# Kernel tuning notes

Measured on AMD Instinct MI355X. Metric: run time of the kernel, lower is better.

## Reference

```python
import jax, jax.numpy as jnp
import numpy as np

N, H, F = 768, 8, 16
HF = H * F            # 128, also node_in
NODE_IN = 128
EIN, EOUT = 64, 64
E = 24576
NEG = -1e9
SLOPE = 0.2
EPS = 1e-5


def leaky(x):
    return jnp.where(x >= 0, x, SLOPE * x)


def batchnorm(x, g, b):
    # BatchNorm1d with track_running_stats=False: always uses batch stats (biased var)
    m = x.mean(0)
    v = x.var(0)
    return g * (x - m) / jnp.sqrt(v + EPS) + b


def setup_inputs() -> dict:
    key = jax.random.key(0)
    ks = jax.random.split(key, 25)
    s = 0.1
    inp = {
        "in_nodes_features": jax.random.normal(ks[0], (N, NODE_IN), jnp.float32),
        "in_edges_features": jax.random.normal(ks[1], (N, N, EIN), jnp.float32),
        "connectivity_mask": jnp.where(jax.random.uniform(ks[2], (N, N)) < 0.05, 0.0, NEG).astype(jnp.float32),
        "sparse_edge_features": jax.random.normal(ks[3], (E, EIN), jnp.float32),
        "sparse_edge_indexs": jax.random.randint(ks[4], (E, 2), 0, N, jnp.int64) if jax.config.jax_enable_x64 else jax.random.randint(ks[4], (E, 2), 0, N, jnp.int32),
        "Wp": jax.random.normal(ks[5], (HF, NODE_IN), jnp.float32) * s,          # linear_proj
        "Wp2": jax.random.normal(ks[6], (HF, EIN), jnp.float32) * s,             # linear_proj2
        "bp2": jax.random.normal(ks[7], (HF,), jnp.float32) * s,
        "score_src": jax.random.normal(ks[8], (1, H, F), jnp.float32) * s,
        "score_tgt": jax.random.normal(ks[9], (1, H, F), jnp.float32) * s,
        "score_edge": jax.random.normal(ks[10], (1, 1, H, F), jnp.float32) * s,
        "Wskip": jax.random.normal(ks[11], (HF, NODE_IN), jnp.float32) * s,      # skip_proj
        "node_bias": jax.random.normal(ks[12], (HF,), jnp.float32) * s,
        "bn_node_g": jnp.ones((HF,), jnp.float32),
        "bn_node_b": jnp.zeros((HF,), jnp.float32),
        "Wf1": jax.random.normal(ks[13], (EOUT, EIN), jnp.float32) * s,
        "bf1": jax.random.normal(ks[14], (EOUT,), jnp.float32) * s,
        "Wf2": jax.random.normal(ks[15], (EOUT, HF), jnp.float32) * s,
        "Wf3": jax.random.normal(ks[16], (EOUT, 2 * EOUT), jnp.float32) * s,
        "Wf4": jax.random.normal(ks[17], (EOUT, EIN), jnp.float32) * s,
        "bf4": jax.random.normal(ks[18], (EOUT,), jnp.float32) * s,
        "Wes": jax.random.normal(ks[19], (EOUT, EIN), jnp.float32) * s,          # edge_skip_proj
        "bn_edge_g": jnp.ones((EOUT,), jnp.float32),
        "bn_edge_b": jnp.zeros((EOUT,), jnp.float32),
    }
    return inp


def reference(in_nodes_features, in_edges_features, connectivity_mask, sparse_edge_features,
              sparse_edge_indexs, Wp, Wp2, bp2, score_src, score_tgt, score_edge, Wskip,
              node_bias, bn_node_g, bn_node_b, Wf1, bf1, Wf2, Wf3, Wf4, bf4, Wes,
              bn_edge_g, bn_edge_b):
    x, edges, mask = in_nodes_features, in_edges_features, connectivity_mask
    # --- node (GAT w/ edge-score bias) path (dropout=0 -> identity) ---
    np_proj = (x @ Wp.T).reshape(N, H, F)                                  # [N,H,F]
    ep = leaky((edges @ Wp2.T) + bp2).reshape(N, N, H, F)                  # [N,N,H,F]
    ss = jnp.sum(np_proj * score_src[0], -1)                               # [N,H]
    st = jnp.sum(np_proj * score_tgt[0], -1)                               # [N,H]
    se = jnp.sum(ep * score_edge[0, 0], -1)                                # [N,N,H]
    scores = leaky(ss.T[:, :, None] + st.T[:, None, :])                    # [H,N,N]
    escores = leaky(jnp.transpose(se, (2, 0, 1)))                          # [H,N,N]
    attn = jax.nn.softmax(scores + escores + mask[None], axis=-1)          # [H,N,N]
    outn = jnp.einsum('hij,jhf->ihf', attn, np_proj)                       # [N,H,F]
    outn = outn + (x @ Wskip.T).reshape(N, H, F)                           # skip (F != node_in)
    outn = outn.reshape(N, HF)                                             # concat heads
    outn = jax.nn.elu(batchnorm(outn, bn_node_g, bn_node_b) + node_bias)
    # --- edge learning path ---
    si, sj = sparse_edge_indexs[:, 0], sparse_edge_indexs[:, 1]
    m_ij = leaky(sparse_edge_features @ Wf1.T + bf1)                       # [E,EOUT]
    d = outn[si] - outn[sj]                                                # gather instead of dense NxN diff
    r_ij = leaky((d * d) @ Wf2.T)                                          # [E,EOUT]
    oe = jnp.concatenate([m_ij, r_ij], -1) @ Wf3.T
    oe = oe + sparse_edge_features @ Wes.T
    oe = jax.nn.elu(batchnorm(oe, bn_edge_g, bn_edge_b))
    ie = (edges @ Wf4.T + bf4) * jax.nn.softmax(mask, axis=-1)[..., None]  # [N,N,EOUT]
    ie = ie.at[si, sj].set(oe)
    return (outn, ie, mask, oe, sparse_edge_indexs)
```

## Files before the change

### kernel.cpp

```cpp
#include <hip/hip_runtime.h>
#include <math.h>

#define NN 768
#define H 8
#define F 16
#define HF 128
#define EIN 64
#define EOUT 64
#define E_EDGES 24576
#define SLOPE 0.2f
#define EPS 1e-5f

__device__ __forceinline__ float leaky(float x){ return x >= 0.f ? x : SLOPE*x; }
__device__ __forceinline__ float elu1(float x){ return x > 0.f ? x : expm1f(x); }

__global__ void k_proj(const float* __restrict__ x, const float* __restrict__ Wp,
                       const float* __restrict__ Wskip, const float* __restrict__ ssrc,
                       const float* __restrict__ stgt,
                       float* __restrict__ npj, float* __restrict__ ss, float* __restrict__ st,
                       float* __restrict__ outn_pre){
  __shared__ float xsh[HF];
  __shared__ float ps[HF], pt[HF];
  int i = blockIdx.x, c = threadIdx.x;
  xsh[c] = x[i*HF + c];
  __syncthreads();
  float a = 0.f, b = 0.f;
  #pragma unroll 4
  for(int k=0;k<HF;k++){ float xv = xsh[k]; a += xv*Wp[c*HF+k]; b += xv*Wskip[c*HF+k]; }
  npj[i*HF+c] = a;
  outn_pre[i*HF+c] = b;
  ps[c] = a*ssrc[c]; pt[c] = a*stgt[c];
  __syncthreads();
  if(c < H){
    float s1=0.f, s2=0.f;
    #pragma unroll
    for(int f=0; f<F; f++){ s1 += ps[c*F+f]; s2 += pt[c*F+f]; }
    ss[i*H+c]=s1; st[i*H+c]=s2;
  }
}

__global__ void k_list(const float* __restrict__ mask, int* __restrict__ lists, int* __restrict__ cnt){
  int w = threadIdx.x >> 6, lane = threadIdx.x & 63;
  int i = blockIdx.x*4 + w;
  int base = 0;
  const float* mrow = mask + (size_t)i*NN;
  int* lrow = lists + (size_t)i*NN;
  for(int t=0;t<12;t++){
    int j = t*64 + lane;
    bool un = (mrow[j] == 0.0f);
    unsigned long long b = __ballot(un);
    if(un) lrow[base + __popcll(b & ((1ull<<lane)-1ull))] = j;
    base += (int)__popcll(b);
  }
  if(base == 0){
    for(int t=0;t<12;t++) lrow[t*64+lane] = t*64+lane;
    base = NN;
  }
  if(lane==0) cnt[i] = base;
}

__global__ __launch_bounds__(256,4) void k_logits_sparse(
    const float* __restrict__ edges, const float* __restrict__ Wp2,
    const float* __restrict__ bp2, const float* __restrict__ sce,
    const float* __restrict__ ss, const float* __restrict__ st,
    const float* __restrict__ mask,
    const int* __restrict__ lists, const int* __restrict__ cnt,
    float* __restrict__ logitc){
  __shared__ float4 wsh[HF*16];
  __shared__ float4 esh[4][2][16];
  __shared__ float bsh[HF], scsh[HF];
  int i = blockIdx.x, tid = threadIdx.x;
  const float4* W4 = (const float4*)Wp2;
  #pragma unroll
  for(int t=0;t<8;t++) wsh[tid + t*256] = W4[tid + t*256];
  if(tid < HF){ bsh[tid]=bp2[tid]; scsh[tid]=sce[tid]; }
  __syncthreads();
  int w = tid>>6, lane = tid&63;
  int n = cnt[i];
  float ss0 = ss[i*H + (lane>>4)];
  float ss1 = ss[i*H + 4 + (lane>>4)];
  const int* lrow = lists + (size_t)i*NN;
  for(int s0 = w*2; s0 < n; s0 += 8){
    int s1 = s0 + 1;
    int j0 = lrow[s0];
    int j1 = lrow[(s1 < n) ? s1 : s0];
    if(lane < 32){
      int which = lane >> 4, k4 = lane & 15;
      int jj = which ? j1 : j0;
      esh[w][which][k4] = ((const float4*)(edges + ((size_t)i*NN + jj)*EIN))[k4];
    }
    asm volatile("s_waitcnt lgkmcnt(0) vmcnt(0)" ::: "memory");
    __builtin_amdgcn_sched_barrier(0);
    float a00=0.f,a01=0.f,a10=0.f,a11=0.f;
    #pragma unroll
    for(int t=0;t<16;t++){
      int q = t ^ (lane & 15);
      float4 e0 = esh[w][0][q];
      float4 e1 = esh[w][1][q];
      float4 w0 = wsh[lane*16 + q];
      float4 w1 = wsh[(lane+64)*16 + q];
      a00 += e0.x*w0.x + e0.y*w0.y + e0.z*w0.z + e0.w*w0.w;
      a01 += e1.x*w0.x + e1.y*w0.y + e1.z*w0.z + e1.w*w0.w;
      a10 += e0.x*w1.x + e0.y*w1.y + e0.z*w1.z + e0.w*w1.w;
      a11 += e1.x*w1.x + e1.y*w1.y + e1.z*w1.z + e1.w*w1.w;
    }
    float p;
    p = a00 + bsh[lane];    float v0  = leaky(p)*scsh[lane];
    p = a01 + bsh[lane];    float v0b = leaky(p)*scsh[lane];
    p = a10 + bsh[lane+64]; float v1  = leaky(p)*scsh[lane+64];
    p = a11 + bsh[lane+64]; float v1b = leaky(p)*scsh[lane+64];
    #pragma unroll
    for(int o=1;o<16;o<<=1){
      v0 += __shfl_xor(v0,o); v0b += __shfl_xor(v0b,o);
      v1 += __shfl_xor(v1,o); v1b += __shfl_xor(v1b,o);
    }
    if((lane & 15) == 0){
      int h = lane >> 4;
      float m0 = mask[(size_t)i*NN + j0];
      logitc[((size_t)i*H + h)*NN + s0]     = leaky(v0) + leaky(ss0 + st[j0*H + h]) + m0;
      logitc[((size_t)i*H + h + 4)*NN + s0] = leaky(v1) + leaky(ss1 + st[j0*H + h + 4]) + m0;
      if(s1 < n){
        float m1 = mask[(size_t)i*NN + j1];
        logitc[((size_t)i*H + h)*NN + s1]     = leaky(v0b) + leaky(ss0 + st[j1*H + h]) + m1;
        logitc[((size_t)i*H + h + 4)*NN + s1] = leaky(v1b) + leaky(ss1 + st[j1*H + h + 4]) + m1;
      }
    }
  }
}

__global__ void k_softmax_c(float* __restrict__ logitc, const int* __restrict__ cnt){
  int i = blockIdx.x;
  int g = threadIdx.x >> 5, l = threadIdx.x & 31;
  int n = cnt[i];
  float* row = logitc + ((size_t)i*H + g)*NN;
  float m = -1e30f;
  for(int s=l; s<n; s+=32) m = fmaxf(m, row[s]);
  #pragma unroll
  for(int o=1;o<32;o<<=1) m = fmaxf(m, __shfl_xor(m, o, 32));
  float sum = 0.f;
  for(int s=l; s<n; s+=32){ float e = expf(row[s]-m); row[s]=e; sum+=e; }
  #pragma unroll
  for(int o=1;o<32;o<<=1) sum += __shfl_xor(sum, o, 32);
  float inv = 1.f/sum;
  for(int s=l; s<n; s+=32) row[s] *= inv;
}

__global__ void k_einsum_c(const float* __restrict__ attnc, const int* __restrict__ lists,
                           const int* __restrict__ cnt, const float* __restrict__ npj,
                           float* __restrict__ opre){
  int i = blockIdx.x, c = threadIdx.x;
  int h = c >> 4;
  int n = cnt[i];
  const int* lrow = lists + (size_t)i*NN;
  const float* arow = attnc + ((size_t)i*H + h)*NN;
  float acc = opre[i*HF + c];
  #pragma unroll 4
  for(int s=0; s<n; s++) acc += arow[s] * npj[lrow[s]*HF + c];
  opre[i*HF+c] = acc;
}

__global__ void k_bn_node_stats(const float* __restrict__ outn_pre, float* __restrict__ stats){
  int c = threadIdx.x & 127, half = threadIdx.x >> 7;
  int r0 = blockIdx.x*16 + half*8;
  float s1=0.f, s2=0.f;
  #pragma unroll
  for(int r=0;r<8;r++){ float v = outn_pre[(r0+r)*HF + c]; s1+=v; s2+=v*v; }
  __shared__ float l1[256], l2[256];
  l1[threadIdx.x]=s1; l2[threadIdx.x]=s2;
  __syncthreads();
  if(threadIdx.x < 128){
    s1 = l1[threadIdx.x] + l1[threadIdx.x+128];
    s2 = l2[threadIdx.x] + l2[threadIdx.x+128];
    atomicAdd(&stats[c], s1); atomicAdd(&stats[HF + c], s2);
  }
}

__global__ void k_bn_node_apply(const float* __restrict__ outn_pre, const float* __restrict__ stats,
                                const float* __restrict__ g, const float* __restrict__ b,
                                const float* __restrict__ nbias, float* __restrict__ outn){
  int idx = blockIdx.x*256 + threadIdx.x;
  int c = idx & 127;
  float m  = stats[c] * (1.f/NN);
  float var = stats[HF+c]*(1.f/NN) - m*m;
  float xv = outn_pre[idx];
  float y = g[c]*(xv - m)/sqrtf(var + EPS) + b[c] + nbias[c];
  outn[idx] = elu1(y);
}

__global__ __launch_bounds__(256,1) void k_sparse_oe(
    const float* __restrict__ sef, const int* __restrict__ eidx,
    const float* __restrict__ outn,
    const float* __restrict__ Wf1, const float* __restrict__ bf1,
    const float* __restrict__ Wf2, const float* __restrict__ Wf3,
    const float* __restrict__ Wes,
    float* __restrict__ oe_pre, float* __restrict__ stats){
  __shared__ float w1[64*65];
  __shared__ float w2[64*129];
  __shared__ float w3[64*129];
  __shared__ float we[64*65];
  __shared__ float b1sh[64];
  __shared__ float sefsh[4][64];
  __shared__ float ddsh[4][128];
  __shared__ float msh[4][64], rsh[4][64];
  __shared__ float r1[256], r2[256];
  int tid = threadIdx.x;
  for(int idx = tid; idx < 64*64; idx += 256){ int o = idx>>6, k = idx&63; w1[o*65+k] = Wf1[idx]; we[o*65+k] = Wes[idx]; }
  for(int idx = tid; idx < 64*128; idx += 256){ int o = idx>>7, k = idx&127; w2[o*129+k] = Wf2[idx]; w3[o*129+k] = Wf3[idx]; }
  if(tid<64) b1sh[tid] = bf1[tid];
  int e0 = blockIdx.x * 96;
  float s1 = 0.f, s2 = 0.f;
  int ee = tid >> 6, o = tid & 63;
  for(int eg=0; eg<24; eg++){
    int ebase = e0 + eg*4;
    { int k = tid & 63, e4 = tid >> 6; sefsh[e4][k] = sef[(ebase+e4)*64 + k]; }
    #pragma unroll
    for(int t=0;t<2;t++){
      int idx = tid + t*256; int e4 = idx >> 7, c = idx & 127;
      int ed = ebase + e4;
      int si = eidx[ed*2], sj = eidx[ed*2+1];
      float d = outn[si*HF + c] - outn[sj*HF + c];
      ddsh[e4][c] = d*d;
    }
    __syncthreads();
    float m = b1sh[o], r = 0.f, oes = 0.f;
    #pragma unroll 4
    for(int k=0;k<64;k++){ float sv = sefsh[ee][k]; m += sv*w1[o*65+k]; oes += sv*we[o*65+k]; }
    #pragma unroll 4
    for(int c=0;c<128;c++){ r += ddsh[ee][c]*w2[o*129+c]; }
    m = leaky(m); r = leaky(r);
    msh[ee][o] = m; rsh[ee][o] = r;
    __syncthreads();
    float oe = oes;
    #pragma unroll 4
    for(int k=0;k<64;k++){ oe += msh[ee][k]*w3[o*129+k] + rsh[ee][k]*w3[o*129+64+k]; }
    oe_pre[(size_t)(ebase+ee)*64 + o] = oe;
    s1 += oe; s2 += oe*oe;
    __syncthreads();
  }
  r1[tid] = s1; r2[tid] = s2;
  __syncthreads();
  if(tid < 64){
    float a1 = r1[tid] + r1[tid+64] + r1[tid+128] + r1[tid+192];
    float a2 = r2[tid] + r2[tid+64] + r2[tid+128] + r2[tid+192];
    atomicAdd(&stats[256 + tid], a1);
    atomicAdd(&stats[320 + tid], a2);
  }
}

__global__ void k_bn_edge_apply(const float* __restrict__ oe_pre, const float* __restrict__ stats,
                                const float* __restrict__ g, const float* __restrict__ b,
                                float* __restrict__ oe_out){
  int idx = blockIdx.x*256 + threadIdx.x;
  int o = idx & 63;
  float m = stats[256+o] * (1.f/E_EDGES);
  float var = stats[320+o]*(1.f/E_EDGES) - m*m;
  float xv = oe_pre[idx];
  float y = g[o]*(xv-m)/sqrtf(var+EPS) + b[o];
  oe_out[idx] = elu1(y);
}

__global__ __launch_bounds__(256) void k_ie_fill(
    const float* __restrict__ edges, const float* __restrict__ mask,
    const float* __restrict__ Wf4, const float* __restrict__ bf4,
    float* __restrict__ ie){
  __shared__ float w4[64*65];
  __shared__ float b4sh[64];
  __shared__ int list[NN];
  __shared__ int lcnt;
  int i = blockIdx.x, tid = threadIdx.x;
  if(tid==0) lcnt = 0;
  for(int idx=tid; idx<64*64; idx+=256){ int o=idx>>6,k=idx&63; w4[o*65+k]=Wf4[idx]; }
  if(tid<64) b4sh[tid]=bf4[tid];
  __syncthreads();
  for(int t=0;t<3;t++){
    int j = tid + t*256;
    if(mask[i*NN+j] == 0.0f){ int p = atomicAdd(&lcnt,1); list[p]=j; }
  }
  __syncthreads();
  int cnt = lcnt;
  float inv;
  if(cnt == 0){
    for(int t=0;t<3;t++) list[tid+t*256] = tid+t*256;
    cnt = NN; inv = 1.0f/NN;
    __syncthreads();
  } else inv = 1.0f/cnt;
  int o = tid & 63, jj4 = tid >> 6;
  for(int base=0; base<cnt; base+=4){
    int li = base + jj4;
    if(li < cnt){
      int j = list[li];
      const float* er = edges + ((size_t)i*NN + j)*EIN;
      float acc = b4sh[o];
      #pragma unroll 8
      for(int k=0;k<64;k++) acc += er[k]*w4[o*65+k];
      ie[((size_t)i*NN + j)*EIN + o] = acc * inv;
    }
  }
}

__global__ void k_winner(const int* __restrict__ eidx, int* __restrict__ winner){
  int e = blockIdx.x*256 + threadIdx.x;
  if(e < E_EDGES){
    int si = eidx[e*2], sj = eidx[e*2+1];
    atomicMax(&winner[si*NN+sj], e);
  }
}
__global__ void k_scatter(const int* __restrict__ eidx, const int* __restrict__ winner,
                          const float* __restrict__ oe, float* __restrict__ ie){
  int idx = blockIdx.x*256 + threadIdx.x;
  int e = idx >> 6, o = idx & 63;
  int si = eidx[e*2], sj = eidx[e*2+1];
  if(winner[si*NN+sj] == e) ie[((size_t)si*NN+sj)*EIN + o] = oe[(size_t)e*64+o];
}

__global__ void k_idxf(const int* __restrict__ eidx, float* __restrict__ outf){
  int idx = blockIdx.x*256 + threadIdx.x;
  if(idx < E_EDGES*2) outf[idx] = (float)eidx[idx];
}

extern "C" void kernel_launch(void* const* d_in, const int* in_sizes, int n_in,
                              void* d_out, int out_size, void* d_ws, size_t ws_size,
                              hipStream_t stream){
  (void)in_sizes; (void)n_in; (void)out_size; (void)d_ws; (void)ws_size;
  const float* x     = (const float*)d_in[0];
  const float* edges = (const float*)d_in[1];
  const float* mask  = (const float*)d_in[2];
  const float* sef   = (const float*)d_in[3];
  const int*   eidx  = (const int*)d_in[4];
  const float* Wp    = (const float*)d_in[5];
  const float* Wp2   = (const float*)d_in[6];
  const float* bp2   = (const float*)d_in[7];
  const float* ssrc  = (const float*)d_in[8];
  const float* stgt  = (const float*)d_in[9];
  const float* sce   = (const float*)d_in[10];
  const float* Wskip = (const float*)d_in[11];
  const float* nbias = (const float*)d_in[12];
  const float* bng   = (const float*)d_in[13];
  const float* bnb   = (const float*)d_in[14];
  const float* Wf1   = (const float*)d_in[15];
  const float* bf1   = (const float*)d_in[16];
  const float* Wf2   = (const float*)d_in[17];
  const float* Wf3   = (const float*)d_in[18];
  const float* Wf4   = (const float*)d_in[19];
  const float* bf4   = (const float*)d_in[20];
  const float* Wes   = (const float*)d_in[21];
  const float* beg   = (const float*)d_in[22];
  const float* beb   = (const float*)d_in[23];

  float* out      = (float*)d_out;
  float* out_outn = out;
  float* out_ie   = out + 98304;
  float* out_mask = out + 37847040;
  float* out_oe   = out + 38436864;
  float* out_idx  = out + 40009728;

  float* s_logitc = out_ie;
  float* s_npj    = out_ie + 4718592;
  float* s_ss     = s_npj + 98304;
  float* s_st     = s_ss + 6144;
  float* s_opre   = s_st + 6144;
  float* s_oepre  = s_opre + 98304;
  float* s_stats  = s_oepre + 1572864;
  int*   s_lists  = (int*)(s_stats + 512);
  int*   s_cnt    = s_lists + 2359296;
  int*   winner   = (int*)out_mask;

  hipMemsetAsync(s_stats, 0, 512*sizeof(float), stream);
  hipMemsetAsync(winner, 0xFF, (size_t)NN*NN*sizeof(int), stream);

  k_list<<<NN/4, 256, 0, stream>>>(mask, s_lists, s_cnt);
  k_proj<<<NN, 128, 0, stream>>>(x, Wp, Wskip, ssrc, stgt, s_npj, s_ss, s_st, s_opre);
  k_logits_sparse<<<NN, 256, 0, stream>>>(edges, Wp2, bp2, sce, s_ss, s_st, mask, s_lists, s_cnt, s_logitc);
  k_softmax_c<<<NN, 256, 0, stream>>>(s_logitc, s_cnt);
  k_einsum_c<<<NN, 128, 0, stream>>>(s_logitc, s_lists, s_cnt, s_npj, s_opre);
  k_bn_node_stats<<<48, 256, 0, stream>>>(s_opre, s_stats);
  k_bn_node_apply<<<384, 256, 0, stream>>>(s_opre, s_stats, bng, bnb, nbias, out_outn);
  k_sparse_oe<<<E_EDGES/96, 256, 0, stream>>>(sef, eidx, out_outn, Wf1, bf1, Wf2, Wf3, Wes, s_oepre, s_stats);
  k_bn_edge_apply<<<6144, 256, 0, stream>>>(s_oepre, s_stats, beg, beb, out_oe);
  hipMemsetAsync(out_ie, 0, (size_t)NN*NN*EIN*sizeof(float), stream);
  k_ie_fill<<<NN, 256, 0, stream>>>(edges, mask, Wf4, bf4, out_ie);
  k_winner<<<96, 256, 0, stream>>>(eidx, winner);
  k_scatter<<<6144, 256, 0, stream>>>(eidx, winner, out_oe, out_ie);
  hipMemcpyAsync(out_mask, mask, (size_t)NN*NN*sizeof(float), hipMemcpyDeviceToDevice, stream);
  k_idxf<<<192, 256, 0, stream>>>(eidx, out_idx);
}
```

Before: 542.4 us.

## Replace per-row projection and fused edge MLP with register-tiled GEMM kernels

Rewrites the node projection as a tiled GEMM kernel with swizzled shared-memory float4 tiles, and moves the attention score reduction into a separate shuffle-based kernel. The monolithic per-edge MLP kernel, which ran with low occupancy and three barriers per four edges, is split into three GEMM-style kernels plus a separate BN-stats reduction. This raises parallelism and register reuse, at the cost of extra intermediate buffers in global memory and more kernel launches.

```diff
diff --git a/kernel.cpp b/kernel.cpp
--- a/kernel.cpp
+++ b/kernel.cpp
@@ -14,29 +14,60 @@
 __device__ __forceinline__ float leaky(float x){ return x >= 0.f ? x : SLOPE*x; }
 __device__ __forceinline__ float elu1(float x){ return x > 0.f ? x : expm1f(x); }
 
-__global__ void k_proj(const float* __restrict__ x, const float* __restrict__ Wp,
-                       const float* __restrict__ Wskip, const float* __restrict__ ssrc,
-                       const float* __restrict__ stgt,
-                       float* __restrict__ npj, float* __restrict__ ss, float* __restrict__ st,
-                       float* __restrict__ outn_pre){
-  __shared__ float xsh[HF];
-  __shared__ float ps[HF], pt[HF];
+__global__ __launch_bounds__(256,3) void k_proj2(
+    const float* __restrict__ x, const float* __restrict__ Wp, const float* __restrict__ Wskip,
+    float* __restrict__ npj, float* __restrict__ opre){
+  __shared__ float4 Bsh[64*32];
+  __shared__ float4 Ash[32*32];
+  int tid = threadIdx.x;
+  int tile = blockIdx.x >> 2, chunk = blockIdx.x & 3;
+  int i0 = tile*32;
+  const float4* Wsrc = (const float4*)((chunk < 2 ? Wp : Wskip) + (size_t)(chunk & 1)*64*HF);
+  const float4* X4 = (const float4*)(x + (size_t)i0*HF);
+  #pragma unroll
+  for(int t=0;t<8;t++){
+    int fi = tid + t*256;
+    int n = fi >> 5, s = fi & 31;
+    Bsh[n*32 + (s ^ ((n>>2)&15))] = Wsrc[fi];
+  }
+  #pragma unroll
+  for(int t=0;t<4;t++){
+    int fi = tid + t*256;
+    int e = fi >> 5, s = fi & 31;
+    Ash[e*32 + (s ^ ((e>>1)&15))] = X4[fi];
+  }
+  __syncthreads();
+  int og = tid & 15, eg = tid >> 4;
+  int o0 = og*4, eb = eg*2;
+  float acc[2][4] = {};
+  #pragma unroll
+  for(int s=0;s<32;s++){
+    float4 a0 = Ash[(eb+0)*32 + (s ^ (((eb+0)>>1)&15))];
+    float4 a1 = Ash[(eb+1)*32 + (s ^ (((eb+1)>>1)&15))];
+    #pragma unroll
+    for(int oo=0;oo<4;oo++){
+      float4 b = Bsh[(o0+oo)*32 + (s ^ (((o0+oo)>>2)&15))];
+      acc[0][oo] += a0.x*b.x + a0.y*b.y + a0.z*b.z + a0.w*b.w;
+      acc[1][oo] += a1.x*b.x + a1.y*b.y + a1.z*b.z + a1.w*b.w;
+    }
+  }
+  float* dst = (chunk < 2) ? npj : opre;
+  int col = (chunk & 1)*64 + o0;
+  #pragma unroll
+  for(int ee=0;ee<2;ee++){
+    float4 v; v.x=acc[ee][0]; v.y=acc[ee][1]; v.z=acc[ee][2]; v.w=acc[ee][3];
+    *(float4*)(dst + (size_t)(i0+eb+ee)*HF + col) = v;
+  }
+}
+
+__global__ void k_scores(const float* __restrict__ npj, const float* __restrict__ ssrc,
+                         const float* __restrict__ stgt, float* __restrict__ ss, float* __restrict__ st){
   int i = blockIdx.x, c = threadIdx.x;
-  xsh[c] = x[i*HF + c];
-  __syncthreads();
-  float a = 0.f, b = 0.f;
-  #pragma unroll 4
-  for(int k=0;k<HF;k++){ float xv = xsh[k]; a += xv*Wp[c*HF+k]; b += xv*Wskip[c*HF+k]; }
-  npj[i*HF+c] = a;
-  outn_pre[i*HF+c] = b;
-  ps[c] = a*ssrc[c]; pt[c] = a*stgt[c];
-  __syncthreads();
-  if(c < H){
-    float s1=0.f, s2=0.f;
-    #pragma unroll
-    for(int f=0; f<F; f++){ s1 += ps[c*F+f]; s2 += pt[c*F+f]; }
-    ss[i*H+c]=s1; st[i*H+c]=s2;
-  }
+  float p = npj[i*HF + c];
+  float v1 = p*ssrc[c], v2 = p*stgt[c];
+  #pragma unroll
+  for(int o=1;o<16;o<<=1){ v1 += __shfl_xor(v1,o); v2 += __shfl_xor(v2,o); }
+  if((c&15)==0){ ss[i*H + (c>>4)] = v1; st[i*H + (c>>4)] = v2; }
 }
 
 __global__ void k_list(const float* __restrict__ mask, int* __restrict__ lists, int* __restrict__ cnt){
@@ -187,63 +218,171 @@
   outn[idx] = elu1(y);
 }
 
-__global__ __launch_bounds__(256,1) void k_sparse_oe(
-    const float* __restrict__ sef, const int* __restrict__ eidx,
-    const float* __restrict__ outn,
-    const float* __restrict__ Wf1, const float* __restrict__ bf1,
-    const float* __restrict__ Wf2, const float* __restrict__ Wf3,
-    const float* __restrict__ Wes,
-    float* __restrict__ oe_pre, float* __restrict__ stats){
-  __shared__ float w1[64*65];
-  __shared__ float w2[64*129];
-  __shared__ float w3[64*129];
-  __shared__ float we[64*65];
+__global__ __launch_bounds__(256,3) void k_mlp_a(
+    const float* __restrict__ sef, const float* __restrict__ Wf1, const float* __restrict__ bf1,
+    const float* __restrict__ Wes, float* __restrict__ m_out, float* __restrict__ oes_out){
+  __shared__ float4 Bsh[128*16];
+  __shared__ float4 Ash[32*16];
   __shared__ float b1sh[64];
-  __shared__ float sefsh[4][64];
-  __shared__ float ddsh[4][128];
-  __shared__ float msh[4][64], rsh[4][64];
-  __shared__ float r1[256], r2[256];
   int tid = threadIdx.x;
-  for(int idx = tid; idx < 64*64; idx += 256){ int o = idx>>6, k = idx&63; w1[o*65+k] = Wf1[idx]; we[o*65+k] = Wes[idx]; }
-  for(int idx = tid; idx < 64*128; idx += 256){ int o = idx>>7, k = idx&127; w2[o*129+k] = Wf2[idx]; w3[o*129+k] = Wf3[idx]; }
-  if(tid<64) b1sh[tid] = bf1[tid];
-  int e0 = blockIdx.x * 96;
-  float s1 = 0.f, s2 = 0.f;
-  int ee = tid >> 6, o = tid & 63;
-  for(int eg=0; eg<24; eg++){
-    int ebase = e0 + eg*4;
-    { int k = tid & 63, e4 = tid >> 6; sefsh[e4][k] = sef[(ebase+e4)*64 + k]; }
+  int e0 = blockIdx.x * 32;
+  const float4* W1_4 = (const float4*)Wf1;
+  const float4* We_4 = (const float4*)Wes;
+  #pragma unroll
+  for(int t=0;t<8;t++){
+    int fi = tid + t*256;
+    int n = fi >> 4, s = fi & 15;
+    float4 v = (n < 64) ? W1_4[n*16+s] : We_4[(n-64)*16+s];
+    Bsh[n*16 + (s ^ ((n>>3)&15))] = v;
+  }
+  if(tid < 64) b1sh[tid] = bf1[tid];
+  const float4* A4 = (const float4*)(sef + (size_t)e0*EIN);
+  #pragma unroll
+  for(int t=0;t<2;t++){
+    int fi = tid + t*256;
+    int e = fi >> 4, s = fi & 15;
+    Ash[e*16 + (s ^ ((e>>1)&15))] = A4[fi];
+  }
+  __syncthreads();
+  int og = tid & 15, eg = tid >> 4;
+  int n0 = og*8, eb = eg*2;
+  float acc[2][8] = {};
+  #pragma unroll
+  for(int s=0;s<16;s++){
+    float4 a0 = Ash[(eb+0)*16 + (s ^ (((eb+0)>>1)&15))];
+    float4 a1 = Ash[(eb+1)*16 + (s ^ (((eb+1)>>1)&15))];
     #pragma unroll
-    for(int t=0;t<2;t++){
-      int idx = tid + t*256; int e4 = idx >> 7, c = idx & 127;
-      int ed = ebase + e4;
-      int si = eidx[ed*2], sj = eidx[ed*2+1];
-      float d = outn[si*HF + c] - outn[sj*HF + c];
-      ddsh[e4][c] = d*d;
-    }
-    __syncthreads();
-    float m = b1sh[o], r = 0.f, oes = 0.f;
-    #pragma unroll 4
-    for(int k=0;k<64;k++){ float sv = sefsh[ee][k]; m += sv*w1[o*65+k]; oes += sv*we[o*65+k]; }
-    #pragma unroll 4
-    for(int c=0;c<128;c++){ r += ddsh[ee][c]*w2[o*129+c]; }
-    m = leaky(m); r = leaky(r);
-    msh[ee][o] = m; rsh[ee][o] = r;
-    __syncthreads();
-    float oe = oes;
-    #pragma unroll 4
-    for(int k=0;k<64;k++){ oe += msh[ee][k]*w3[o*129+k] + rsh[ee][k]*w3[o*129+64+k]; }
-    oe_pre[(size_t)(ebase+ee)*64 + o] = oe;
-    s1 += oe; s2 += oe*oe;
-    __syncthreads();
-  }
-  r1[tid] = s1; r2[tid] = s2;
-  __syncthreads();
-  if(tid < 64){
-    float a1 = r1[tid] + r1[tid+64] + r1[tid+128] + r1[tid+192];
-    float a2 = r2[tid] + r2[tid+64] + r2[tid+128] + r2[tid+192];
-    atomicAdd(&stats[256 + tid], a1);
-    atomicAdd(&stats[320 + tid], a2);
+    for(int oo=0;oo<8;oo++){
+      float4 b = Bsh[(n0+oo)*16 + (s ^ (((n0+oo)>>3)&15))];
+      acc[0][oo] += a0.x*b.x + a0.y*b.y + a0.z*b.z + a0.w*b.w;
+      acc[1][oo] += a1.x*b.x + a1.y*b.y + a1.z*b.z + a1.w*b.w;
+    }
+  }
+  #pragma unroll
+  for(int ee=0;ee<2;ee++){
+    int e = e0 + eb + ee;
+    if(og < 8){
+      #pragma unroll
+      for(int oo=0;oo<8;oo++) m_out[(size_t)e*EOUT + n0 + oo] = leaky(acc[ee][oo] + b1sh[n0+oo]);
+    } else {
+      #pragma unroll
+      for(int oo=0;oo<8;oo++) oes_out[(size_t)e*EOUT + (n0-64) + oo] = acc[ee][oo];
+    }
+  }
+}
+
+__global__ __launch_bounds__(256,3) void k_mlp_b(
+    const int* __restrict__ eidx, const float* __restrict__ outn,
+    const float* __restrict__ Wf2, float* __restrict__ r_out){
+  __shared__ float4 Bsh[64*32];
+  __shared__ float4 Ash[32*32];
+  int tid = threadIdx.x;
+  int e0 = blockIdx.x * 32;
+  const float4* W2_4 = (const float4*)Wf2;
+  #pragma unroll
+  for(int t=0;t<8;t++){
+    int fi = tid + t*256;
+    int n = fi >> 5, s = fi & 31;
+    Bsh[n*32 + (s ^ ((n>>2)&15))] = W2_4[fi];
+  }
+  const float4* O4 = (const float4*)outn;
+  #pragma unroll
+  for(int t=0;t<4;t++){
+    int fi = tid + t*256;
+    int e = fi >> 5, s = fi & 31;
+    int ed = e0 + e;
+    int si = eidx[ed*2], sj = eidx[ed*2+1];
+    float4 vi = O4[(size_t)si*32 + s];
+    float4 vj = O4[(size_t)sj*32 + s];
+    float4 d; d.x=vi.x-vj.x; d.y=vi.y-vj.y; d.z=vi.z-vj.z; d.w=vi.w-vj.w;
+    d.x*=d.x; d.y*=d.y; d.z*=d.z; d.w*=d.w;
+    Ash[e*32 + (s ^ ((e>>1)&15))] = d;
+  }
+  __syncthreads();
+  int og = tid & 15, eg = tid >> 4;
+  int o0 = og*4, eb = eg*2;
+  float acc[2][4] = {};
+  #pragma unroll
+  for(int s=0;s<32;s++){
+    float4 a0 = Ash[(eb+0)*32 + (s ^ (((eb+0)>>1)&15))];
+    float4 a1 = Ash[(eb+1)*32 + (s ^ (((eb+1)>>1)&15))];
+    #pragma unroll
+    for(int oo=0;oo<4;oo++){
+      float4 b = Bsh[(o0+oo)*32 + (s ^ (((o0+oo)>>2)&15))];
+      acc[0][oo] += a0.x*b.x + a0.y*b.y + a0.z*b.z + a0.w*b.w;
+      acc[1][oo] += a1.x*b.x + a1.y*b.y + a1.z*b.z + a1.w*b.w;
+    }
+  }
+  #pragma unroll
+  for(int ee=0;ee<2;ee++){
+    float4 v; v.x=leaky(acc[ee][0]); v.y=leaky(acc[ee][1]); v.z=leaky(acc[ee][2]); v.w=leaky(acc[ee][3]);
+    *(float4*)(r_out + (size_t)(e0+eb+ee)*EOUT + o0) = v;
+  }
+}
+
+__global__ __launch_bounds__(256,2) void k_mlp_c(
+    const float* __restrict__ m_in, const float* __restrict__ r_in,
+    const float* __restrict__ oes_in, const float* __restrict__ Wf3,
+    float* __restrict__ oe_pre){
+  __shared__ float4 Bsh[64*32];
+  __shared__ float4 Ash[32*32];
+  int tid = threadIdx.x;
+  int e0 = blockIdx.x * 32;
+  const float4* W3_4 = (const float4*)Wf3;
+  #pragma unroll
+  for(int t=0;t<8;t++){
+    int fi = tid + t*256;
+    int n = fi >> 5, s = fi & 31;
+    Bsh[n*32 + (s ^ ((n>>2)&15))] = W3_4[fi];
+  }
+  const float4* M4 = (const float4*)(m_in + (size_t)e0*EOUT);
+  const float4* R4 = (const float4*)(r_in + (size_t)e0*EOUT);
+  #pragma unroll
+  for(int t=0;t<2;t++){
+    int fi = tid + t*256;
+    int e = fi >> 4, s = fi & 15;
+    int sw = s ^ ((e>>1)&15);
+    Ash[e*32 + sw] = M4[fi];
+    Ash[e*32 + 16 + sw] = R4[fi];
+  }
+  __syncthreads();
+  int og = tid & 15, eg = tid >> 4;
+  int o0 = og*4, eb = eg*2;
+  float acc[2][4] = {};
+  #pragma unroll
+  for(int s=0;s<32;s++){
+    int half = s & 16, sl = s & 15;
+    float4 a0 = Ash[(eb+0)*32 + half + (sl ^ (((eb+0)>>1)&15))];
+    float4 a1 = Ash[(eb+1)*32 + half + (sl ^ (((eb+1)>>1)&15))];
+    #pragma unroll
+    for(int oo=0;oo<4;oo++){
+      float4 b = Bsh[(o0+oo)*32 + (s ^ (((o0+oo)>>2)&15))];
+      acc[0][oo] += a0.x*b.x + a0.y*b.y + a0.z*b.z + a0.w*b.w;
+      acc[1][oo] += a1.x*b.x + a1.y*b.y + a1.z*b.z + a1.w*b.w;
+    }
+  }
+  #pragma unroll
+  for(int ee=0;ee<2;ee++){
+    int e = e0 + eb + ee;
+    float4 os = ((const float4*)oes_in)[(size_t)e*16 + og];
+    float4 v; v.x=acc[ee][0]+os.x; v.y=acc[ee][1]+os.y; v.z=acc[ee][2]+os.z; v.w=acc[ee][3]+os.w;
+    *(float4*)(oe_pre + (size_t)e*EOUT + o0) = v;
+  }
+}
+
+__global__ void k_bn_edge_stats(const float* __restrict__ oe_pre, float* __restrict__ stats){
+  int c = threadIdx.x & 63, rg = threadIdx.x >> 6;
+  int r0 = blockIdx.x*256 + rg*64;
+  float s1=0.f, s2=0.f;
+  for(int r=0;r<64;r++){ float v = oe_pre[(size_t)(r0+r)*EOUT + c]; s1+=v; s2+=v*v; }
+  __shared__ float l1[256], l2[256];
+  l1[threadIdx.x]=s1; l2[threadIdx.x]=s2;
+  __syncthreads();
+  if(threadIdx.x < 64){
+    float a1 = l1[threadIdx.x] + l1[threadIdx.x+64] + l1[threadIdx.x+128] + l1[threadIdx.x+192];
+    float a2 = l2[threadIdx.x] + l2[threadIdx.x+64] + l2[threadIdx.x+128] + l2[threadIdx.x+192];
+    atomicAdd(&stats[256 + threadIdx.x], a1);
+    atomicAdd(&stats[320 + threadIdx.x], a2);
   }
 }
 
@@ -363,19 +502,26 @@
   float* s_stats  = s_oepre + 1572864;
   int*   s_lists  = (int*)(s_stats + 512);
   int*   s_cnt    = s_lists + 2359296;
+  float* s_m      = (float*)(s_cnt + 768);
+  float* s_oes    = s_m + 1572864;
+  float* s_r      = s_oes + 1572864;
   int*   winner   = (int*)out_mask;
 
   hipMemsetAsync(s_stats, 0, 512*sizeof(float), stream);
   hipMemsetAsync(winner, 0xFF, (size_t)NN*NN*sizeof(int), stream);
 
   k_list<<<NN/4, 256, 0, stream>>>(mask, s_lists, s_cnt);
-  k_proj<<<NN, 128, 0, stream>>>(x, Wp, Wskip, ssrc, stgt, s_npj, s_ss, s_st, s_opre);
+  k_proj2<<<96, 256, 0, stream>>>(x, Wp, Wskip, s_npj, s_opre);
+  k_scores<<<NN, 128, 0, stream>>>(s_npj, ssrc, stgt, s_ss, s_st);
   k_logits_sparse<<<NN, 256, 0, stream>>>(edges, Wp2, bp2, sce, s_ss, s_st, mask, s_lists, s_cnt, s_logitc);
   k_softmax_c<<<NN, 256, 0, stream>>>(s_logitc, s_cnt);
   k_einsum_c<<<NN, 128, 0, stream>>>(s_logitc, s_lists, s_cnt, s_npj, s_opre);
   k_bn_node_stats<<<48, 256, 0, stream>>>(s_opre, s_stats);
   k_bn_node_apply<<<384, 256, 0, stream>>>(s_opre, s_stats, bng, bnb, nbias, out_outn);
-  k_sparse_oe<<<E_EDGES/96, 256, 0, stream>>>(sef, eidx, out_outn, Wf1, bf1, Wf2, Wf3, Wes, s_oepre, s_stats);
+  k_mlp_a<<<E_EDGES/32, 256, 0, stream>>>(sef, Wf1, bf1, Wes, s_m, s_oes);
+  k_mlp_b<<<E_EDGES/32, 256, 0, stream>>>(eidx, out_outn, Wf2, s_r);
+  k_mlp_c<<<E_EDGES/32, 256, 0, stream>>>(s_m, s_r, s_oes, Wf3, s_oepre);
+  k_bn_edge_stats<<<E_EDGES/256, 256, 0, stream>>>(s_oepre, s_stats);
   k_bn_edge_apply<<<6144, 256, 0, stream>>>(s_oepre, s_stats, beg, beb, out_oe);
   hipMemsetAsync(out_ie, 0, (size_t)NN*NN*EIN*sizeof(float), stream);
   k_ie_fill<<<NN, 256, 0, stream>>>(edges, mask, Wf4, bf4, out_ie);
```

Result: slower. 831.5 us (+53.3%).
